# Kernel tuning notes

Hardware: AMD Instinct MI355X
Metric: run time of the kernel (lower is better)

## Reference

```python
import jax, jax.numpy as jnp
import numpy as np

D_MODEL = 1024
N_HEADS = 16
SEQ = 2048
BATCH = 2


def setup_inputs() -> dict:
    key = jax.random.key(0)
    ks = jax.random.split(key, 12)
    s = 1.0 / np.sqrt(D_MODEL)
    return {
        "q_input": jax.random.normal(ks[0], (BATCH, SEQ, D_MODEL), jnp.float32),
        "k_input": jax.random.normal(ks[1], (BATCH, SEQ, D_MODEL), jnp.float32),
        "v_input": jax.random.normal(ks[2], (BATCH, SEQ, D_MODEL), jnp.float32),
        "key_padding_mask": jnp.zeros((BATCH, SEQ), dtype=bool),
        "wq": jax.random.normal(ks[3], (D_MODEL, D_MODEL), jnp.float32) * s,
        "bq": jnp.zeros((D_MODEL,), jnp.float32),
        "wk": jax.random.normal(ks[4], (D_MODEL, D_MODEL), jnp.float32) * s,
        "bk": jnp.zeros((D_MODEL,), jnp.float32),
        "wv": jax.random.normal(ks[5], (D_MODEL, D_MODEL), jnp.float32) * s,
        "bv": jnp.zeros((D_MODEL,), jnp.float32),
        "wo": jax.random.normal(ks[6], (D_MODEL, D_MODEL), jnp.float32) * s,
        "bo": jnp.zeros((D_MODEL,), jnp.float32),
    }


def reference(q_input, k_input, v_input, key_padding_mask, wq, bq, wk, bk, wv, bv, wo, bo):
    B, Lq, _ = q_input.shape
    Lk = k_input.shape[1]
    d_head = D_MODEL // N_HEADS
    # torch Linear: x @ W.T + b
    Q = q_input @ wq.T + bq
    K = k_input @ wk.T + bk
    V = v_input @ wv.T + bv
    # [B, H, L, d_head]
    Qh = Q.reshape(B, Lq, N_HEADS, d_head).transpose(0, 2, 1, 3)
    Kh = K.reshape(B, Lk, N_HEADS, d_head).transpose(0, 2, 1, 3)
    Vh = V.reshape(B, Lk, N_HEADS, d_head).transpose(0, 2, 1, 3)
    scores = jnp.einsum("bhqd,bhkd->bhqk", Qh, Kh) / jnp.sqrt(jnp.float32(d_head))
    # causal mask (use_mask=True)
    causal = jnp.arange(Lk)[None, :] > jnp.arange(Lq)[:, None]  # [Lq, Lk]
    scores = jnp.where(causal[None, None], -jnp.inf, scores)
    # key padding mask [B,1,1,Lk]
    scores = jnp.where(key_padding_mask[:, None, None, :], -jnp.inf, scores)
    # module's global all-inf fallback (scalar condition)
    probs = jnp.where(
        jnp.all(jnp.isinf(scores)),
        jnp.full_like(scores, 1.0 / Lk),
        jax.nn.softmax(scores, axis=-1),
    )
    # dropout is identity in eval mode
    out = jnp.einsum("bhqk,bhkd->bhqd", probs, Vh)
    out = out.transpose(0, 2, 1, 3).reshape(B, Lq, D_MODEL)
    return out @ wo.T + bo
```

## Files before the change

### kernel.cpp

```cpp
#include <hip/hip_runtime.h>
#include <cstdint>
#include <cstddef>

#define DM   1024
#define HEADS 16
#define DH    64
#define SEQL  2048
#define BATCH 2
#define MTOT  (BATCH*SEQL)

typedef __attribute__((ext_vector_type(8))) short short8;
typedef __attribute__((ext_vector_type(4))) float floatx4;

__device__ __forceinline__ unsigned short f2bf(float f) {
  unsigned int u = __float_as_uint(f);
  u = (u + 0x7FFFu + ((u >> 16) & 1u)) >> 16;
  return (unsigned short)u;
}

__device__ __forceinline__ void async_ld16(const void* g, void* l) {
  __builtin_amdgcn_global_load_lds(
      (const __attribute__((address_space(1))) unsigned int*)g,
      (__attribute__((address_space(3))) unsigned int*)l, 16, 0, 0);
}

__global__ void cvt_all(const float* __restrict__ q, const float* __restrict__ k,
                        const float* __restrict__ v, const float* __restrict__ w0,
                        const float* __restrict__ w1, const float* __restrict__ w2,
                        const float* __restrict__ w3,
                        unsigned short* __restrict__ Xq, unsigned short* __restrict__ Xk,
                        unsigned short* __restrict__ Xv, unsigned short* __restrict__ W0,
                        unsigned short* __restrict__ W1, unsigned short* __restrict__ W2,
                        unsigned short* __restrict__ W3) {
  const int bid = blockIdx.x;
  const float* src; unsigned short* dst; int base;
  if (bid < 12288) {
    int seg = bid >> 12;
    base = (bid & 4095) * 1024;
    src = seg == 0 ? q : seg == 1 ? k : v;
    dst = seg == 0 ? Xq : seg == 1 ? Xk : Xv;
  } else {
    int b2 = bid - 12288;
    int seg = b2 >> 10;
    base = (b2 & 1023) * 1024;
    src = seg == 0 ? w0 : seg == 1 ? w1 : seg == 2 ? w2 : w3;
    dst = seg == 0 ? W0 : seg == 1 ? W1 : seg == 2 ? W2 : W3;
  }
  int i = base + threadIdx.x * 4;
  float4 vv = *(const float4*)(src + i);
  ushort4 o;
  o.x = f2bf(vv.x); o.y = f2bf(vv.y); o.z = f2bf(vv.z); o.w = f2bf(vv.w);
  *(ushort4*)(dst + i) = o;
}

__global__ __launch_bounds__(256, 3) void qkv_gemm(
    const unsigned short* Xq, const unsigned short* Xk, const unsigned short* Xv,
    const unsigned short* Wq, const unsigned short* Wk, const unsigned short* Wv,
    const float* bq, const float* bk, const float* bv,
    unsigned short* Qo, unsigned short* Ko, unsigned short* Vo) {
  __shared__ unsigned short As[128 * 64], Bs[128 * 64];
  const unsigned short *A, *Bw; const float* bias; unsigned short* Cout;
  if (blockIdx.z == 0)      { A = Xq; Bw = Wq; bias = bq; Cout = Qo; }
  else if (blockIdx.z == 1) { A = Xk; Bw = Wk; bias = bk; Cout = Ko; }
  else                      { A = Xv; Bw = Wv; bias = bv; Cout = Vo; }

  const int K = DM, N = DM;
  const int m0 = blockIdx.y * 128, n0 = blockIdx.x * 128;
  const int tid  = threadIdx.x;
  const int lane = tid & 63, wvi = tid >> 6;
  const int lq = lane & 15, quad = lane >> 4;
  const int wrow = wvi >> 1, wcol = wvi & 1;

  floatx4 acc[4][4];
  #pragma unroll
  for (int i = 0; i < 4; i++)
    #pragma unroll
    for (int j = 0; j < 4; j++)
      #pragma unroll
      for (int e = 0; e < 4; e++) acc[i][j][e] = 0.0f;

  for (int kt = 0; kt < K; kt += 64) {
    #pragma unroll
    for (int cc = 0; cc < 4; cc++) {
      int c = wvi + cc * 4;
      int e = c * 512 + lane * 8;
      int r = e >> 6, col = e & 63;
      async_ld16(A  + (size_t)(m0 + r) * K + kt + col, As + c * 512);
      async_ld16(Bw + (size_t)(n0 + r) * K + kt + col, Bs + c * 512);
    }
    __syncthreads();
    #pragma unroll
    for (int ks = 0; ks < 64; ks += 32) {
      short8 af[4], bf[4];
      #pragma unroll
      for (int i = 0; i < 4; i++)
        af[i] = *(const short8*)&As[(wrow * 64 + i * 16 + lq) * 64 + ks + quad * 8];
      #pragma unroll
      for (int j = 0; j < 4; j++)
        bf[j] = *(const short8*)&Bs[(wcol * 64 + j * 16 + lq) * 64 + ks + quad * 8];
      #pragma unroll
      for (int i = 0; i < 4; i++)
        #pragma unroll
        for (int j = 0; j < 4; j++)
          acc[i][j] = __builtin_amdgcn_mfma_f32_16x16x32_bf16(af[i], bf[j], acc[i][j], 0, 0, 0);
    }
    __syncthreads();
  }

  #pragma unroll
  for (int i = 0; i < 4; i++) {
    #pragma unroll
    for (int j = 0; j < 4; j++) {
      int colg = n0 + wcol * 64 + j * 16 + lq;
      float bb = bias[colg];
      #pragma unroll
      for (int r = 0; r < 4; r++) {
        int rowg = m0 + wrow * 64 + i * 16 + quad * 4 + r;
        ((unsigned short*)Cout)[(size_t)rowg * N + colg] = f2bf(acc[i][j][r] + bb);
      }
    }
  }
}

__global__ __launch_bounds__(256, 4) void out_gemm(
    const unsigned short* __restrict__ A, const unsigned short* __restrict__ Bw,
    const float* __restrict__ bias, float* __restrict__ C) {
  __shared__ unsigned short As[128 * 64], Bs[64 * 64];
  const int K = DM, N = DM;
  const int m0 = blockIdx.y * 128, n0 = blockIdx.x * 64;
  const int tid  = threadIdx.x;
  const int lane = tid & 63, wvi = tid >> 6;
  const int lq = lane & 15, quad = lane >> 4;
  const int wrow = wvi >> 1, wcol = wvi & 1;

  floatx4 acc[4][2];
  #pragma unroll
  for (int i = 0; i < 4; i++)
    #pragma unroll
    for (int j = 0; j < 2; j++)
      #pragma unroll
      for (int e = 0; e < 4; e++) acc[i][j][e] = 0.0f;

  for (int kt = 0; kt < K; kt += 64) {
    #pragma unroll
    for (int cc = 0; cc < 4; cc++) {
      int c = wvi + cc * 4;
      int e = c * 512 + lane * 8;
      int r = e >> 6, col = e & 63;
      async_ld16(A + (size_t)(m0 + r) * K + kt + col, As + c * 512);
    }
    #pragma unroll
    for (int cc = 0; cc < 2; cc++) {
      int c = wvi + cc * 4;
      int e = c * 512 + lane * 8;
      int r = e >> 6, col = e & 63;
      async_ld16(Bw + (size_t)(n0 + r) * K + kt + col, Bs + c * 512);
    }
    __syncthreads();
    #pragma unroll
    for (int ks = 0; ks < 64; ks += 32) {
      short8 af[4], bf[2];
      #pragma unroll
      for (int i = 0; i < 4; i++)
        af[i] = *(const short8*)&As[(wrow * 64 + i * 16 + lq) * 64 + ks + quad * 8];
      #pragma unroll
      for (int j = 0; j < 2; j++)
        bf[j] = *(const short8*)&Bs[(wcol * 32 + j * 16 + lq) * 64 + ks + quad * 8];
      #pragma unroll
      for (int i = 0; i < 4; i++)
        #pragma unroll
        for (int j = 0; j < 2; j++)
          acc[i][j] = __builtin_amdgcn_mfma_f32_16x16x32_bf16(af[i], bf[j], acc[i][j], 0, 0, 0);
    }
    __syncthreads();
  }

  #pragma unroll
  for (int i = 0; i < 4; i++) {
    #pragma unroll
    for (int j = 0; j < 2; j++) {
      int colg = n0 + wcol * 32 + j * 16 + lq;
      float bb = bias[colg];
      #pragma unroll
      for (int r = 0; r < 4; r++) {
        int rowg = m0 + wrow * 64 + i * 16 + quad * 4 + r;
        C[(size_t)rowg * N + colg] = acc[i][j][r] + bb;
      }
    }
  }
}

__global__ void v_transpose(const unsigned short* __restrict__ Vb,
                            unsigned short* __restrict__ VT) {
  __shared__ unsigned short Ts[64 * 72];
  const int kt = blockIdx.x, h = blockIdx.y, b = blockIdx.z;
  const int tid = threadIdx.x;
  const int krow = tid >> 4, dcol = (tid & 15) * 4;
  const unsigned short* src = Vb + (size_t)(b * SEQL + kt * 64) * DM + h * DH;
  #pragma unroll
  for (int j = 0; j < 4; j++) {
    ushort4 v = *(const ushort4*)(src + (size_t)(j * 16 + krow) * DM + dcol);
    Ts[(dcol + 0) * 72 + j * 16 + krow] = v.x;
    Ts[(dcol + 1) * 72 + j * 16 + krow] = v.y;
    Ts[(dcol + 2) * 72 + j * 16 + krow] = v.z;
    Ts[(dcol + 3) * 72 + j * 16 + krow] = v.w;
  }
  __syncthreads();
  unsigned short* dst = VT + (size_t)((b * HEADS + h) * 32 + kt) * 4096;
  #pragma unroll
  for (int jj = 0; jj < 2; jj++) {
    int e = jj * 256 + tid;
    int drow = e >> 3, koff = (e & 7) * 8;
    *(short8*)(dst + drow * 64 + koff) = *(const short8*)&Ts[drow * 72 + koff];
  }
}

__global__ __launch_bounds__(256, 4) void attn_kernel(
    const unsigned short* __restrict__ Q, const unsigned short* __restrict__ K,
    const unsigned short* __restrict__ VT, const unsigned char* __restrict__ kpm,
    unsigned short* __restrict__ O) {
  __shared__ unsigned short Ks[64 * 72];
  __shared__ unsigned short VTs[64 * 72];
  __shared__ unsigned short Ps[4][16 * 72];

  const int bid = blockIdx.x;
  const int qt = 31 - (bid >> 5);
  const int bh = bid & 31;
  const int h = bh & 15, b = bh >> 4;
  const int tid = threadIdx.x, lane = tid & 63, wvi = tid >> 6;
  const int lq = lane & 15, quad = lane >> 4;
  const size_t bbase = (size_t)b * SEQL * DM;

  const int srow = tid >> 4;
  const int scol = (tid & 15) * 4;

  const unsigned short* kptr = K + bbase + (size_t)h * DH + (size_t)srow * DM + scol;
  const unsigned short* vptr = VT + (size_t)(b * HEADS + h) * 32 * 4096 + srow * 64 + scol;
  const unsigned char*  mptr = kpm + (size_t)b * SEQL + quad * 4;

  const unsigned short* Qrow = Q + bbase + (size_t)(qt * 64 + wvi * 16 + lq) * DM + h * DH;
  const short8 qf0 = *(const short8*)(Qrow + quad * 8);
  const short8 qf1 = *(const short8*)(Qrow + 32 + quad * 8);

  ushort4 kr[4], vr[4];
  unsigned int mr[4];
  #pragma unroll
  for (int j = 0; j < 4; j++) {
    kr[j] = *(const ushort4*)(kptr + (size_t)j * 16 * DM);
    vr[j] = *(const ushort4*)(vptr + j * 1024);
  }
  #pragma unroll
  for (int t = 0; t < 4; t++) mr[t] = *(const unsigned int*)(mptr + t * 16);
  kptr += (size_t)64 * DM; vptr += 4096; mptr += 64;

  float l_run = 0.f;
  floatx4 o[4];
  #pragma unroll
  for (int t = 0; t < 4; t++)
    #pragma unroll
    for (int e = 0; e < 4; e++) o[t][e] = 0.f;

  const float SC = 0.125f * 1.44269504088896f;
  const float C0 = -24.0f * SC;
  const int qg = wvi * 16 + lq;

  auto tile_body = [&](bool diag, const unsigned int* mcur) {
    floatx4 st[4];
    #pragma unroll
    for (int t = 0; t < 4; t++) {
      #pragma unroll
      for (int e = 0; e < 4; e++) st[t][e] = 0.f;
      const short8 a0 = *(const short8*)&Ks[(t * 16 + lq) * 72 + quad * 8];
      const short8 a1 = *(const short8*)&Ks[(t * 16 + lq) * 72 + 32 + quad * 8];
      st[t] = __builtin_amdgcn_mfma_f32_16x16x32_bf16(a0, qf0, st[t], 0, 0, 0);
      st[t] = __builtin_amdgcn_mfma_f32_16x16x32_bf16(a1, qf1, st[t], 0, 0, 0);
    }

    float x[4][4];
    #pragma unroll
    for (int t = 0; t < 4; t++)
      #pragma unroll
      for (int r = 0; r < 4; r++) x[t][r] = st[t][r];

    if (__any((int)((mcur[0] | mcur[1] | mcur[2] | mcur[3]) != 0u))) {
      #pragma unroll
      for (int t = 0; t < 4; t++)
        #pragma unroll
        for (int r = 0; r < 4; r++)
          if ((mcur[t] >> (8 * r)) & 0xffu) x[t][r] = -1e33f;
    }
    if (diag) {
      #pragma unroll
      for (int t = 0; t < 4; t++)
        #pragma unroll
        for (int r = 0; r < 4; r++)
          if (t * 16 + quad * 4 + r > qg) x[t][r] = -1e33f;
    }

    #pragma unroll
    for (int t = 0; t < 4; t++)
      #pragma unroll
      for (int r = 0; r < 4; r++) {
        const float p = exp2f(fmaf(x[t][r], SC, C0));
        x[t][r] = p;
        l_run += p;
      }

    #pragma unroll
    for (int t = 0; t < 4; t++) {
      unsigned int p01 = (__float_as_uint(x[t][1]) & 0xffff0000u) | (__float_as_uint(x[t][0]) >> 16);
      unsigned int p23 = (__float_as_uint(x[t][3]) & 0xffff0000u) | (__float_as_uint(x[t][2]) >> 16);
      *(uint2*)&Ps[wvi][lq * 72 + t * 16 + quad * 4] = make_uint2(p01, p23);
    }

    const short8 pa0 = *(const short8*)&Ps[wvi][lq * 72 + quad * 8];
    const short8 pa1 = *(const short8*)&Ps[wvi][lq * 72 + 32 + quad * 8];
    #pragma unroll
    for (int t = 0; t < 4; t++) {
      const short8 b0 = *(const short8*)&VTs[(t * 16 + lq) * 72 + quad * 8];
      const short8 b1 = *(const short8*)&VTs[(t * 16 + lq) * 72 + 32 + quad * 8];
      o[t] = __builtin_amdgcn_mfma_f32_16x16x32_bf16(pa0, b0, o[t], 0, 0, 0);
      o[t] = __builtin_amdgcn_mfma_f32_16x16x32_bf16(pa1, b1, o[t], 0, 0, 0);
    }
  };

  for (int kt = 0; kt < qt; kt++) {
    __syncthreads();
    #pragma unroll
    for (int j = 0; j < 4; j++) {
      *(ushort4*)&Ks [(j * 16 + srow) * 72 + scol] = kr[j];
      *(ushort4*)&VTs[(j * 16 + srow) * 72 + scol] = vr[j];
    }
    unsigned int mcur[4];
    #pragma unroll
    for (int t = 0; t < 4; t++) mcur[t] = mr[t];
    __syncthreads();

    #pragma unroll
    for (int j = 0; j < 4; j++) {
      kr[j] = *(const ushort4*)(kptr + (size_t)j * 16 * DM);
      vr[j] = *(const ushort4*)(vptr + j * 1024);
    }
    #pragma unroll
    for (int t = 0; t < 4; t++) mr[t] = *(const unsigned int*)(mptr + t * 16);
    kptr += (size_t)64 * DM; vptr += 4096; mptr += 64;

    tile_body(false, mcur);
  }

  __syncthreads();
  #pragma unroll
  for (int j = 0; j < 4; j++) {
    *(ushort4*)&Ks [(j * 16 + srow) * 72 + scol] = kr[j];
    *(ushort4*)&VTs[(j * 16 + srow) * 72 + scol] = vr[j];
  }
  __syncthreads();
  tile_body(true, mr);

  l_run += __shfl_xor(l_run, 16);
  l_run += __shfl_xor(l_run, 32);
  const float li = 1.0f / l_run;
  float linv[4];
  #pragma unroll
  for (int r = 0; r < 4; r++) linv[r] = __shfl(li, quad * 20 + r);
  #pragma unroll
  for (int t = 0; t < 4; t++)
    #pragma unroll
    for (int r = 0; r < 4; r++) {
      const int rowg = qt * 64 + wvi * 16 + quad * 4 + r;
      const int colg = h * 64 + t * 16 + lq;
      O[bbase + (size_t)rowg * DM + colg] = f2bf(o[t][r] * linv[r]);
    }
}

extern "C" void kernel_launch(void* const* d_in, const int* in_sizes, int n_in,
                              void* d_out, int out_size, void* d_ws, size_t ws_size,
                              hipStream_t stream) {
  const float* qin = (const float*)d_in[0];
  const float* kin = (const float*)d_in[1];
  const float* vin = (const float*)d_in[2];
  const unsigned char* kpm = (const unsigned char*)d_in[3];
  const float* wq = (const float*)d_in[4];
  const float* bq = (const float*)d_in[5];
  const float* wk = (const float*)d_in[6];
  const float* bk = (const float*)d_in[7];
  const float* wv = (const float*)d_in[8];
  const float* bv = (const float*)d_in[9];
  const float* wo = (const float*)d_in[10];
  const float* bo = (const float*)d_in[11];

  const size_t XN = (size_t)MTOT * DM;
  const size_t WN = (size_t)DM * DM;
  unsigned short* Xq  = (unsigned short*)d_ws;
  unsigned short* Xk  = Xq  + XN;
  unsigned short* Xv  = Xk  + XN;
  unsigned short* Wqb = Xv  + XN;
  unsigned short* Wkb = Wqb + WN;
  unsigned short* Wvb = Wkb + WN;
  unsigned short* Wob = Wvb + WN;
  unsigned short* Qb  = Wob + WN;
  unsigned short* Kb  = Qb  + XN;
  unsigned short* Vb  = Kb  + XN;
  unsigned short* Ob  = Vb  + XN;
  unsigned short* VTg = Xq;

  cvt_all<<<dim3(16384), 256, 0, stream>>>(qin, kin, vin, wq, wk, wv, wo,
                                           Xq, Xk, Xv, Wqb, Wkb, Wvb, Wob);

  dim3 g1(DM / 128, MTOT / 128, 3);
  qkv_gemm<<<g1, 256, 0, stream>>>(Xq, Xk, Xv, Wqb, Wkb, Wvb, bq, bk, bv, Qb, Kb, Vb);

  v_transpose<<<dim3(SEQL / 64, HEADS, BATCH), 256, 0, stream>>>(Vb, VTg);

  attn_kernel<<<dim3(BATCH * HEADS * (SEQL / 64)), 256, 0, stream>>>(Qb, Kb, VTg, kpm, Ob);

  dim3 g2(DM / 64, MTOT / 128, 1);
  out_gemm<<<g2, 256, 0, stream>>>(Ob, Wob, bo, (float*)d_out);
}
```

Measured before the change: 226.0 us.

## Fuse V transpose into QKV GEMM epilogue and process two query tiles per attention block

The QKV GEMM epilogue now writes V directly in the per-head transposed tile layout, which removes the separate v_transpose kernel and its extra round trip through global memory. The attention kernel now handles 128 query rows per block as two 64-row sub-tiles that share each staged K/V tile, halving K/V reloads and the grid size. Query-tile scheduling is remapped to a 16-tile pairing order. In exchange, the V epilogue does scattered 8-byte stores, and the attention kernel needs more accumulator registers, which may lower occupancy.

```diff
diff --git a/kernel.cpp b/kernel.cpp
--- a/kernel.cpp
+++ b/kernel.cpp
@@ -57,12 +57,12 @@
     const unsigned short* Xq, const unsigned short* Xk, const unsigned short* Xv,
     const unsigned short* Wq, const unsigned short* Wk, const unsigned short* Wv,
     const float* bq, const float* bk, const float* bv,
-    unsigned short* Qo, unsigned short* Ko, unsigned short* Vo) {
+    unsigned short* Qo, unsigned short* Ko, unsigned short* VTo) {
   __shared__ unsigned short As[128 * 64], Bs[128 * 64];
   const unsigned short *A, *Bw; const float* bias; unsigned short* Cout;
   if (blockIdx.z == 0)      { A = Xq; Bw = Wq; bias = bq; Cout = Qo; }
   else if (blockIdx.z == 1) { A = Xk; Bw = Wk; bias = bk; Cout = Ko; }
-  else                      { A = Xv; Bw = Wv; bias = bv; Cout = Vo; }
+  else                      { A = Xv; Bw = Wv; bias = bv; Cout = VTo; }
 
   const int K = DM, N = DM;
   const int m0 = blockIdx.y * 128, n0 = blockIdx.x * 128;
@@ -107,16 +107,38 @@
     __syncthreads();
   }
 
-  #pragma unroll
-  for (int i = 0; i < 4; i++) {
-    #pragma unroll
-    for (int j = 0; j < 4; j++) {
-      int colg = n0 + wcol * 64 + j * 16 + lq;
-      float bb = bias[colg];
-      #pragma unroll
-      for (int r = 0; r < 4; r++) {
-        int rowg = m0 + wrow * 64 + i * 16 + quad * 4 + r;
-        ((unsigned short*)Cout)[(size_t)rowg * N + colg] = f2bf(acc[i][j][r] + bb);
+  if (blockIdx.z == 2) {
+    #pragma unroll
+    for (int i = 0; i < 4; i++) {
+      const int rowg = m0 + wrow * 64 + i * 16 + quad * 4;
+      const int bb  = rowg >> 11;
+      const int kt2 = (rowg & 2047) >> 6;
+      const int k0  = rowg & 63;
+      #pragma unroll
+      for (int j = 0; j < 4; j++) {
+        const int colg = n0 + wcol * 64 + j * 16 + lq;
+        const int h2 = colg >> 6, d2 = colg & 63;
+        const float bb_v = bias[colg];
+        ushort4 w;
+        w.x = f2bf(acc[i][j][0] + bb_v);
+        w.y = f2bf(acc[i][j][1] + bb_v);
+        w.z = f2bf(acc[i][j][2] + bb_v);
+        w.w = f2bf(acc[i][j][3] + bb_v);
+        *(ushort4*)(Cout + (size_t)((bb * HEADS + h2) * 32 + kt2) * 4096 + d2 * 64 + k0) = w;
+      }
+    }
+  } else {
+    #pragma unroll
+    for (int i = 0; i < 4; i++) {
+      #pragma unroll
+      for (int j = 0; j < 4; j++) {
+        int colg = n0 + wcol * 64 + j * 16 + lq;
+        float bb = bias[colg];
+        #pragma unroll
+        for (int r = 0; r < 4; r++) {
+          int rowg = m0 + wrow * 64 + i * 16 + quad * 4 + r;
+          Cout[(size_t)rowg * N + colg] = f2bf(acc[i][j][r] + bb);
+        }
       }
     }
   }
@@ -190,31 +212,6 @@
   }
 }
 
-__global__ void v_transpose(const unsigned short* __restrict__ Vb,
-                            unsigned short* __restrict__ VT) {
-  __shared__ unsigned short Ts[64 * 72];
-  const int kt = blockIdx.x, h = blockIdx.y, b = blockIdx.z;
-  const int tid = threadIdx.x;
-  const int krow = tid >> 4, dcol = (tid & 15) * 4;
-  const unsigned short* src = Vb + (size_t)(b * SEQL + kt * 64) * DM + h * DH;
-  #pragma unroll
-  for (int j = 0; j < 4; j++) {
-    ushort4 v = *(const ushort4*)(src + (size_t)(j * 16 + krow) * DM + dcol);
-    Ts[(dcol + 0) * 72 + j * 16 + krow] = v.x;
-    Ts[(dcol + 1) * 72 + j * 16 + krow] = v.y;
-    Ts[(dcol + 2) * 72 + j * 16 + krow] = v.z;
-    Ts[(dcol + 3) * 72 + j * 16 + krow] = v.w;
-  }
-  __syncthreads();
-  unsigned short* dst = VT + (size_t)((b * HEADS + h) * 32 + kt) * 4096;
-  #pragma unroll
-  for (int jj = 0; jj < 2; jj++) {
-    int e = jj * 256 + tid;
-    int drow = e >> 3, koff = (e & 7) * 8;
-    *(short8*)(dst + drow * 64 + koff) = *(const short8*)&Ts[drow * 72 + koff];
-  }
-}
-
 __global__ __launch_bounds__(256, 4) void attn_kernel(
     const unsigned short* __restrict__ Q, const unsigned short* __restrict__ K,
     const unsigned short* __restrict__ VT, const unsigned char* __restrict__ kpm,
@@ -224,7 +221,8 @@
   __shared__ unsigned short Ps[4][16 * 72];
 
   const int bid = blockIdx.x;
-  const int qt = 31 - (bid >> 5);
+  const int g = bid >> 5;
+  const int qt = (g < 8) ? (15 - g) : (g - 8);
   const int bh = bid & 31;
   const int h = bh & 15, b = bh >> 4;
   const int tid = threadIdx.x, lane = tid & 63, wvi = tid >> 6;
@@ -238,9 +236,14 @@
   const unsigned short* vptr = VT + (size_t)(b * HEADS + h) * 32 * 4096 + srow * 64 + scol;
   const unsigned char*  mptr = kpm + (size_t)b * SEQL + quad * 4;
 
-  const unsigned short* Qrow = Q + bbase + (size_t)(qt * 64 + wvi * 16 + lq) * DM + h * DH;
-  const short8 qf0 = *(const short8*)(Qrow + quad * 8);
-  const short8 qf1 = *(const short8*)(Qrow + 32 + quad * 8);
+  const unsigned short* QrowA = Q + bbase + (size_t)(qt * 128 + wvi * 16 + lq) * DM + h * DH;
+  const short8 qfA0 = *(const short8*)(QrowA + quad * 8);
+  const short8 qfA1 = *(const short8*)(QrowA + 32 + quad * 8);
+  const unsigned short* QrowB = QrowA + (size_t)64 * DM;
+  const short8 qfB0 = *(const short8*)(QrowB + quad * 8);
+  const short8 qfB1 = *(const short8*)(QrowB + 32 + quad * 8);
+
+  const int nk = 2 * qt + 2;
 
   ushort4 kr[4], vr[4];
   unsigned int mr[4];
@@ -253,123 +256,131 @@
   for (int t = 0; t < 4; t++) mr[t] = *(const unsigned int*)(mptr + t * 16);
   kptr += (size_t)64 * DM; vptr += 4096; mptr += 64;
 
-  float l_run = 0.f;
-  floatx4 o[4];
+  float lA = 0.f, lB = 0.f;
+  floatx4 oA[4], oB[4];
   #pragma unroll
   for (int t = 0; t < 4; t++)
     #pragma unroll
-    for (int e = 0; e < 4; e++) o[t][e] = 0.f;
+    for (int e = 0; e < 4; e++) { oA[t][e] = 0.f; oB[t][e] = 0.f; }
 
   const float SC = 0.125f * 1.44269504088896f;
   const float C0 = -24.0f * SC;
   const int qg = wvi * 16 + lq;
 
-  auto tile_body = [&](bool diag, const unsigned int* mcur) {
-    floatx4 st[4];
+  for (int kt = 0; kt < nk; kt++) {
+    __syncthreads();
+    #pragma unroll
+    for (int j = 0; j < 4; j++) {
+      *(ushort4*)&Ks [(j * 16 + srow) * 72 + scol] = kr[j];
+      *(ushort4*)&VTs[(j * 16 + srow) * 72 + scol] = vr[j];
+    }
+    unsigned int mcur[4];
+    #pragma unroll
+    for (int t = 0; t < 4; t++) mcur[t] = mr[t];
+    __syncthreads();
+
+    if (kt + 1 < nk) {
+      #pragma unroll
+      for (int j = 0; j < 4; j++) {
+        kr[j] = *(const ushort4*)(kptr + (size_t)j * 16 * DM);
+        vr[j] = *(const ushort4*)(vptr + j * 1024);
+      }
+      #pragma unroll
+      for (int t = 0; t < 4; t++) mr[t] = *(const unsigned int*)(mptr + t * 16);
+      kptr += (size_t)64 * DM; vptr += 4096; mptr += 64;
+    }
+
+    floatx4 sA[4], sB[4];
     #pragma unroll
     for (int t = 0; t < 4; t++) {
       #pragma unroll
-      for (int e = 0; e < 4; e++) st[t][e] = 0.f;
+      for (int e = 0; e < 4; e++) { sA[t][e] = 0.f; sB[t][e] = 0.f; }
       const short8 a0 = *(const short8*)&Ks[(t * 16 + lq) * 72 + quad * 8];
       const short8 a1 = *(const short8*)&Ks[(t * 16 + lq) * 72 + 32 + quad * 8];
-      st[t] = __builtin_amdgcn_mfma_f32_16x16x32_bf16(a0, qf0, st[t], 0, 0, 0);
-      st[t] = __builtin_amdgcn_mfma_f32_16x16x32_bf16(a1, qf1, st[t], 0, 0, 0);
-    }
-
-    float x[4][4];
+      sA[t] = __builtin_amdgcn_mfma_f32_16x16x32_bf16(a0, qfA0, sA[t], 0, 0, 0);
+      sA[t] = __builtin_amdgcn_mfma_f32_16x16x32_bf16(a1, qfA1, sA[t], 0, 0, 0);
+      sB[t] = __builtin_amdgcn_mfma_f32_16x16x32_bf16(a0, qfB0, sB[t], 0, 0, 0);
+      sB[t] = __builtin_amdgcn_mfma_f32_16x16x32_bf16(a1, qfB1, sB[t], 0, 0, 0);
+    }
+
+    if (__any((int)((mcur[0] | mcur[1] | mcur[2] | mcur[3]) != 0u))) {
+      #pragma unroll
+      for (int t = 0; t < 4; t++)
+        #pragma unroll
+        for (int r = 0; r < 4; r++)
+          if ((mcur[t] >> (8 * r)) & 0xffu) { sA[t][r] = -1e33f; sB[t][r] = -1e33f; }
+    }
+    if (kt >= 2 * qt) {
+      const int offA = qg + (2 * qt - kt) * 64;
+      #pragma unroll
+      for (int t = 0; t < 4; t++)
+        #pragma unroll
+        for (int r = 0; r < 4; r++)
+          if (t * 16 + quad * 4 + r > offA) sA[t][r] = -1e33f;
+    }
+    if (kt == 2 * qt + 1) {
+      #pragma unroll
+      for (int t = 0; t < 4; t++)
+        #pragma unroll
+        for (int r = 0; r < 4; r++)
+          if (t * 16 + quad * 4 + r > qg) sB[t][r] = -1e33f;
+    }
+
     #pragma unroll
     for (int t = 0; t < 4; t++)
       #pragma unroll
-      for (int r = 0; r < 4; r++) x[t][r] = st[t][r];
-
-    if (__any((int)((mcur[0] | mcur[1] | mcur[2] | mcur[3]) != 0u))) {
-      #pragma unroll
-      for (int t = 0; t < 4; t++)
-        #pragma unroll
-        for (int r = 0; r < 4; r++)
-          if ((mcur[t] >> (8 * r)) & 0xffu) x[t][r] = -1e33f;
-    }
-    if (diag) {
-      #pragma unroll
-      for (int t = 0; t < 4; t++)
-        #pragma unroll
-        for (int r = 0; r < 4; r++)
-          if (t * 16 + quad * 4 + r > qg) x[t][r] = -1e33f;
-    }
-
-    #pragma unroll
-    for (int t = 0; t < 4; t++)
-      #pragma unroll
       for (int r = 0; r < 4; r++) {
-        const float p = exp2f(fmaf(x[t][r], SC, C0));
-        x[t][r] = p;
-        l_run += p;
+        const float pA = exp2f(fmaf(sA[t][r], SC, C0));
+        const float pB = exp2f(fmaf(sB[t][r], SC, C0));
+        sA[t][r] = pA; lA += pA;
+        sB[t][r] = pB; lB += pB;
       }
 
     #pragma unroll
     for (int t = 0; t < 4; t++) {
-      unsigned int p01 = (__float_as_uint(x[t][1]) & 0xffff0000u) | (__float_as_uint(x[t][0]) >> 16);
-      unsigned int p23 = (__float_as_uint(x[t][3]) & 0xffff0000u) | (__float_as_uint(x[t][2]) >> 16);
+      unsigned int p01 = (__float_as_uint(sA[t][1]) & 0xffff0000u) | (__float_as_uint(sA[t][0]) >> 16);
+      unsigned int p23 = (__float_as_uint(sA[t][3]) & 0xffff0000u) | (__float_as_uint(sA[t][2]) >> 16);
       *(uint2*)&Ps[wvi][lq * 72 + t * 16 + quad * 4] = make_uint2(p01, p23);
     }
-
-    const short8 pa0 = *(const short8*)&Ps[wvi][lq * 72 + quad * 8];
-    const short8 pa1 = *(const short8*)&Ps[wvi][lq * 72 + 32 + quad * 8];
+    const short8 paA0 = *(const short8*)&Ps[wvi][lq * 72 + quad * 8];
+    const short8 paA1 = *(const short8*)&Ps[wvi][lq * 72 + 32 + quad * 8];
+    #pragma unroll
+    for (int t = 0; t < 4; t++) {
+      unsigned int p01 = (__float_as_uint(sB[t][1]) & 0xffff0000u) | (__float_as_uint(sB[t][0]) >> 16);
+      unsigned int p23 = (__float_as_uint(sB[t][3]) & 0xffff0000u) | (__float_as_uint(sB[t][2]) >> 16);
+      *(uint2*)&Ps[wvi][lq * 72 + t * 16 + quad * 4] = make_uint2(p01, p23);
+    }
+    const short8 paB0 = *(const short8*)&Ps[wvi][lq * 72 + quad * 8];
+    const short8 paB1 = *(const short8*)&Ps[wvi][lq * 72 + 32 + quad * 8];
+
     #pragma unroll
     for (int t = 0; t < 4; t++) {
       const short8 b0 = *(const short8*)&VTs[(t * 16 + lq) * 72 + quad * 8];
       const short8 b1 = *(const short8*)&VTs[(t * 16 + lq) * 72 + 32 + quad * 8];
-      o[t] = __builtin_amdgcn_mfma_f32_16x16x32_bf16(pa0, b0, o[t], 0, 0, 0);
-      o[t] = __builtin_amdgcn_mfma_f32_16x16x32_bf16(pa1, b1, o[t], 0, 0, 0);
-    }
-  };
-
-  for (int kt = 0; kt < qt; kt++) {
-    __syncthreads();
-    #pragma unroll
-    for (int j = 0; j < 4; j++) {
-      *(ushort4*)&Ks [(j * 16 + srow) * 72 + scol] = kr[j];
-      *(ushort4*)&VTs[(j * 16 + srow) * 72 + scol] = vr[j];
-    }
-    unsigned int mcur[4];
-    #pragma unroll
-    for (int t = 0; t < 4; t++) mcur[t] = mr[t];
-    __syncthreads();
-
-    #pragma unroll
-    for (int j = 0; j < 4; j++) {
-      kr[j] = *(const ushort4*)(kptr + (size_t)j * 16 * DM);
-      vr[j] = *(const ushort4*)(vptr + j * 1024);
-    }
-    #pragma unroll
-    for (int t = 0; t < 4; t++) mr[t] = *(const unsigned int*)(mptr + t * 16);
-    kptr += (size_t)64 * DM; vptr += 4096; mptr += 64;
-
-    tile_body(false, mcur);
-  }
-
-  __syncthreads();
-  #pragma unroll
-  for (int j = 0; j < 4; j++) {
-    *(ushort4*)&Ks [(j * 16 + srow) * 72 + scol] = kr[j];
-    *(ushort4*)&VTs[(j * 16 + srow) * 72 + scol] = vr[j];
-  }
-  __syncthreads();
-  tile_body(true, mr);
-
-  l_run += __shfl_xor(l_run, 16);
-  l_run += __shfl_xor(l_run, 32);
-  const float li = 1.0f / l_run;
-  float linv[4];
-  #pragma unroll
-  for (int r = 0; r < 4; r++) linv[r] = __shfl(li, quad * 20 + r);
+      oA[t] = __builtin_amdgcn_mfma_f32_16x16x32_bf16(paA0, b0, oA[t], 0, 0, 0);
+      oA[t] = __builtin_amdgcn_mfma_f32_16x16x32_bf16(paA1, b1, oA[t], 0, 0, 0);
+      oB[t] = __builtin_amdgcn_mfma_f32_16x16x32_bf16(paB0, b0, oB[t], 0, 0, 0);
+      oB[t] = __builtin_amdgcn_mfma_f32_16x16x32_bf16(paB1, b1, oB[t], 0, 0, 0);
+    }
+  }
+
+  lA += __shfl_xor(lA, 16); lA += __shfl_xor(lA, 32);
+  lB += __shfl_xor(lB, 16); lB += __shfl_xor(lB, 32);
+  const float liA = 1.0f / lA, liB = 1.0f / lB;
+  float invA[4], invB[4];
+  #pragma unroll
+  for (int r = 0; r < 4; r++) {
+    invA[r] = __shfl(liA, quad * 20 + r);
+    invB[r] = __shfl(liB, quad * 20 + r);
+  }
   #pragma unroll
   for (int t = 0; t < 4; t++)
     #pragma unroll
     for (int r = 0; r < 4; r++) {
-      const int rowg = qt * 64 + wvi * 16 + quad * 4 + r;
+      const int rowA = qt * 128 + wvi * 16 + quad * 4 + r;
       const int colg = h * 64 + t * 16 + lq;
-      O[bbase + (size_t)rowg * DM + colg] = f2bf(o[t][r] * linv[r]);
+      O[bbase + (size_t)rowA * DM + colg] = f2bf(oA[t][r] * invA[r]);
+      O[bbase + (size_t)(rowA + 64) * DM + colg] = f2bf(oB[t][r] * invB[r]);
     }
 }
 
@@ -400,19 +411,16 @@
   unsigned short* Wob = Wvb + WN;
   unsigned short* Qb  = Wob + WN;
   unsigned short* Kb  = Qb  + XN;
-  unsigned short* Vb  = Kb  + XN;
-  unsigned short* Ob  = Vb  + XN;
-  unsigned short* VTg = Xq;
+  unsigned short* VTg = Kb  + XN;
+  unsigned short* Ob  = VTg + XN;
 
   cvt_all<<<dim3(16384), 256, 0, stream>>>(qin, kin, vin, wq, wk, wv, wo,
                                            Xq, Xk, Xv, Wqb, Wkb, Wvb, Wob);
 
   dim3 g1(DM / 128, MTOT / 128, 3);
-  qkv_gemm<<<g1, 256, 0, stream>>>(Xq, Xk, Xv, Wqb, Wkb, Wvb, bq, bk, bv, Qb, Kb, Vb);
-
-  v_transpose<<<dim3(SEQL / 64, HEADS, BATCH), 256, 0, stream>>>(Vb, VTg);
-
-  attn_kernel<<<dim3(BATCH * HEADS * (SEQL / 64)), 256, 0, stream>>>(Qb, Kb, VTg, kpm, Ob);
+  qkv_gemm<<<g1, 256, 0, stream>>>(Xq, Xk, Xv, Wqb, Wkb, Wvb, bq, bk, bv, Qb, Kb, VTg);
+
+  attn_kernel<<<dim3(BATCH * HEADS * (SEQL / 128)), 256, 0, stream>>>(Qb, Kb, VTg, kpm, Ob);
 
   dim3 g2(DM / 64, MTOT / 128, 1);
   out_gemm<<<g2, 256, 0, stream>>>(Ob, Wob, bo, (float*)d_out);
```

Result: slower. 247.6 us (+9.6%).

## Fuse activation bf16 conversion and V transpose into QKV GEMM

Applied to the files above, without the earlier changes.

Removes the separate fp32-to-bf16 conversion pass over the Q/K/V activations. The QKV GEMM now loads fp32 rows directly, rounds them to bf16 in registers and writes them to shared memory. The V projection epilogue writes straight into the transposed per-head tile layout, so the v_transpose kernel is dropped. This cuts global memory traffic and two launches, but A-tile loads become synchronous register loads instead of async LDS loads, and the rounding changes from round-to-nearest-even to round-half-up.

```diff
diff --git a/kernel.cpp b/kernel.cpp
--- a/kernel.cpp
+++ b/kernel.cpp
@@ -24,28 +24,15 @@
       (__attribute__((address_space(3))) unsigned int*)l, 16, 0, 0);
 }
 
-__global__ void cvt_all(const float* __restrict__ q, const float* __restrict__ k,
-                        const float* __restrict__ v, const float* __restrict__ w0,
-                        const float* __restrict__ w1, const float* __restrict__ w2,
-                        const float* __restrict__ w3,
-                        unsigned short* __restrict__ Xq, unsigned short* __restrict__ Xk,
-                        unsigned short* __restrict__ Xv, unsigned short* __restrict__ W0,
-                        unsigned short* __restrict__ W1, unsigned short* __restrict__ W2,
-                        unsigned short* __restrict__ W3) {
+__global__ void cvt_w(const float* __restrict__ w0, const float* __restrict__ w1,
+                      const float* __restrict__ w2, const float* __restrict__ w3,
+                      unsigned short* __restrict__ W0, unsigned short* __restrict__ W1,
+                      unsigned short* __restrict__ W2, unsigned short* __restrict__ W3) {
   const int bid = blockIdx.x;
-  const float* src; unsigned short* dst; int base;
-  if (bid < 12288) {
-    int seg = bid >> 12;
-    base = (bid & 4095) * 1024;
-    src = seg == 0 ? q : seg == 1 ? k : v;
-    dst = seg == 0 ? Xq : seg == 1 ? Xk : Xv;
-  } else {
-    int b2 = bid - 12288;
-    int seg = b2 >> 10;
-    base = (b2 & 1023) * 1024;
-    src = seg == 0 ? w0 : seg == 1 ? w1 : seg == 2 ? w2 : w3;
-    dst = seg == 0 ? W0 : seg == 1 ? W1 : seg == 2 ? W2 : W3;
-  }
+  const int seg = bid >> 10;
+  const int base = (bid & 1023) * 1024;
+  const float* src = seg == 0 ? w0 : seg == 1 ? w1 : seg == 2 ? w2 : w3;
+  unsigned short* dst = seg == 0 ? W0 : seg == 1 ? W1 : seg == 2 ? W2 : W3;
   int i = base + threadIdx.x * 4;
   float4 vv = *(const float4*)(src + i);
   ushort4 o;
@@ -54,15 +41,15 @@
 }
 
 __global__ __launch_bounds__(256, 3) void qkv_gemm(
-    const unsigned short* Xq, const unsigned short* Xk, const unsigned short* Xv,
+    const float* Xq, const float* Xk, const float* Xv,
     const unsigned short* Wq, const unsigned short* Wk, const unsigned short* Wv,
     const float* bq, const float* bk, const float* bv,
-    unsigned short* Qo, unsigned short* Ko, unsigned short* Vo) {
+    unsigned short* Qo, unsigned short* Ko, unsigned short* VTo) {
   __shared__ unsigned short As[128 * 64], Bs[128 * 64];
-  const unsigned short *A, *Bw; const float* bias; unsigned short* Cout;
+  const float* A; const unsigned short* Bw; const float* bias; unsigned short* Cout;
   if (blockIdx.z == 0)      { A = Xq; Bw = Wq; bias = bq; Cout = Qo; }
   else if (blockIdx.z == 1) { A = Xk; Bw = Wk; bias = bk; Cout = Ko; }
-  else                      { A = Xv; Bw = Wv; bias = bv; Cout = Vo; }
+  else                      { A = Xv; Bw = Wv; bias = bv; Cout = VTo; }
 
   const int K = DM, N = DM;
   const int m0 = blockIdx.y * 128, n0 = blockIdx.x * 128;
@@ -71,6 +58,9 @@
   const int lq = lane & 15, quad = lane >> 4;
   const int wrow = wvi >> 1, wcol = wvi & 1;
 
+  const int arow8 = lane >> 3;
+  const int acol  = (lane & 7) * 8;
+
   floatx4 acc[4][4];
   #pragma unroll
   for (int i = 0; i < 4; i++)
@@ -85,8 +75,29 @@
       int c = wvi + cc * 4;
       int e = c * 512 + lane * 8;
       int r = e >> 6, col = e & 63;
-      async_ld16(A  + (size_t)(m0 + r) * K + kt + col, As + c * 512);
       async_ld16(Bw + (size_t)(n0 + r) * K + kt + col, Bs + c * 512);
+    }
+    #pragma unroll
+    for (int cc = 0; cc < 4; cc++) {
+      int c = wvi + cc * 4;
+      int r = c * 8 + arow8;
+      const float* src = A + (size_t)(m0 + r) * K + kt + acol;
+      float4 f0 = *(const float4*)src;
+      float4 f1 = *(const float4*)(src + 4);
+      unsigned int a0 = __float_as_uint(f0.x) + 0x8000u;
+      unsigned int a1 = __float_as_uint(f0.y) + 0x8000u;
+      unsigned int a2 = __float_as_uint(f0.z) + 0x8000u;
+      unsigned int a3 = __float_as_uint(f0.w) + 0x8000u;
+      unsigned int a4 = __float_as_uint(f1.x) + 0x8000u;
+      unsigned int a5 = __float_as_uint(f1.y) + 0x8000u;
+      unsigned int a6 = __float_as_uint(f1.z) + 0x8000u;
+      unsigned int a7 = __float_as_uint(f1.w) + 0x8000u;
+      uint4 w;
+      w.x = (a1 & 0xffff0000u) | (a0 >> 16);
+      w.y = (a3 & 0xffff0000u) | (a2 >> 16);
+      w.z = (a5 & 0xffff0000u) | (a4 >> 16);
+      w.w = (a7 & 0xffff0000u) | (a6 >> 16);
+      *(uint4*)&As[c * 512 + lane * 8] = w;
     }
     __syncthreads();
     #pragma unroll
@@ -107,16 +118,38 @@
     __syncthreads();
   }
 
-  #pragma unroll
-  for (int i = 0; i < 4; i++) {
-    #pragma unroll
-    for (int j = 0; j < 4; j++) {
-      int colg = n0 + wcol * 64 + j * 16 + lq;
-      float bb = bias[colg];
-      #pragma unroll
-      for (int r = 0; r < 4; r++) {
-        int rowg = m0 + wrow * 64 + i * 16 + quad * 4 + r;
-        ((unsigned short*)Cout)[(size_t)rowg * N + colg] = f2bf(acc[i][j][r] + bb);
+  if (blockIdx.z == 2) {
+    #pragma unroll
+    for (int i = 0; i < 4; i++) {
+      const int rowg = m0 + wrow * 64 + i * 16 + quad * 4;
+      const int bb  = rowg >> 11;
+      const int kt2 = (rowg & 2047) >> 6;
+      const int k0  = rowg & 63;
+      #pragma unroll
+      for (int j = 0; j < 4; j++) {
+        const int colg = n0 + wcol * 64 + j * 16 + lq;
+        const int h2 = colg >> 6, d2 = colg & 63;
+        const float bb_v = bias[colg];
+        ushort4 w;
+        w.x = f2bf(acc[i][j][0] + bb_v);
+        w.y = f2bf(acc[i][j][1] + bb_v);
+        w.z = f2bf(acc[i][j][2] + bb_v);
+        w.w = f2bf(acc[i][j][3] + bb_v);
+        *(ushort4*)(Cout + (size_t)((bb * HEADS + h2) * 32 + kt2) * 4096 + d2 * 64 + k0) = w;
+      }
+    }
+  } else {
+    #pragma unroll
+    for (int i = 0; i < 4; i++) {
+      #pragma unroll
+      for (int j = 0; j < 4; j++) {
+        int colg = n0 + wcol * 64 + j * 16 + lq;
+        float bb = bias[colg];
+        #pragma unroll
+        for (int r = 0; r < 4; r++) {
+          int rowg = m0 + wrow * 64 + i * 16 + quad * 4 + r;
+          Cout[(size_t)rowg * N + colg] = f2bf(acc[i][j][r] + bb);
+        }
       }
     }
   }
@@ -187,31 +220,6 @@
         C[(size_t)rowg * N + colg] = acc[i][j][r] + bb;
       }
     }
-  }
-}
-
-__global__ void v_transpose(const unsigned short* __restrict__ Vb,
-                            unsigned short* __restrict__ VT) {
-  __shared__ unsigned short Ts[64 * 72];
-  const int kt = blockIdx.x, h = blockIdx.y, b = blockIdx.z;
-  const int tid = threadIdx.x;
-  const int krow = tid >> 4, dcol = (tid & 15) * 4;
-  const unsigned short* src = Vb + (size_t)(b * SEQL + kt * 64) * DM + h * DH;
-  #pragma unroll
-  for (int j = 0; j < 4; j++) {
-    ushort4 v = *(const ushort4*)(src + (size_t)(j * 16 + krow) * DM + dcol);
-    Ts[(dcol + 0) * 72 + j * 16 + krow] = v.x;
-    Ts[(dcol + 1) * 72 + j * 16 + krow] = v.y;
-    Ts[(dcol + 2) * 72 + j * 16 + krow] = v.z;
-    Ts[(dcol + 3) * 72 + j * 16 + krow] = v.w;
-  }
-  __syncthreads();
-  unsigned short* dst = VT + (size_t)((b * HEADS + h) * 32 + kt) * 4096;
-  #pragma unroll
-  for (int jj = 0; jj < 2; jj++) {
-    int e = jj * 256 + tid;
-    int drow = e >> 3, koff = (e & 7) * 8;
-    *(short8*)(dst + drow * 64 + koff) = *(const short8*)&Ts[drow * 72 + koff];
   }
 }
 
@@ -391,26 +399,19 @@
 
   const size_t XN = (size_t)MTOT * DM;
   const size_t WN = (size_t)DM * DM;
-  unsigned short* Xq  = (unsigned short*)d_ws;
-  unsigned short* Xk  = Xq  + XN;
-  unsigned short* Xv  = Xk  + XN;
-  unsigned short* Wqb = Xv  + XN;
+  unsigned short* Wqb = (unsigned short*)d_ws;
   unsigned short* Wkb = Wqb + WN;
   unsigned short* Wvb = Wkb + WN;
   unsigned short* Wob = Wvb + WN;
   unsigned short* Qb  = Wob + WN;
   unsigned short* Kb  = Qb  + XN;
-  unsigned short* Vb  = Kb  + XN;
-  unsigned short* Ob  = Vb  + XN;
-  unsigned short* VTg = Xq;
-
-  cvt_all<<<dim3(16384), 256, 0, stream>>>(qin, kin, vin, wq, wk, wv, wo,
-                                           Xq, Xk, Xv, Wqb, Wkb, Wvb, Wob);
+  unsigned short* VTg = Kb  + XN;
+  unsigned short* Ob  = VTg + XN;
+
+  cvt_w<<<dim3(4096), 256, 0, stream>>>(wq, wk, wv, wo, Wqb, Wkb, Wvb, Wob);
 
   dim3 g1(DM / 128, MTOT / 128, 3);
-  qkv_gemm<<<g1, 256, 0, stream>>>(Xq, Xk, Xv, Wqb, Wkb, Wvb, bq, bk, bv, Qb, Kb, Vb);
-
-  v_transpose<<<dim3(SEQL / 64, HEADS, BATCH), 256, 0, stream>>>(Vb, VTg);
+  qkv_gemm<<<g1, 256, 0, stream>>>(qin, kin, vin, Wqb, Wkb, Wvb, bq, bk, bv, Qb, Kb, VTg);
 
   attn_kernel<<<dim3(BATCH * HEADS * (SEQL / 64)), 256, 0, stream>>>(Qb, Kb, VTg, kpm, Ob);
 
```

Result: slower. 238.2 us (+5.4%).

## Fuse V transpose into QKV GEMM epilogue and retile output GEMM

Applied to the files above, without the earlier changes.

The QKV GEMM now writes V directly in the per-head transposed tile layout the attention kernel expects, which removes the separate v_transpose kernel and its extra read and write of V. The output projection GEMM is retiled from 128x64 to 64x128 blocks, with each wave owning 16 rows across all 128 columns. The fused epilogue writes 4-element chunks with a strided scatter, which may coalesce less well than row-major stores.

```diff
diff --git a/kernel.cpp b/kernel.cpp
--- a/kernel.cpp
+++ b/kernel.cpp
@@ -57,12 +57,12 @@
     const unsigned short* Xq, const unsigned short* Xk, const unsigned short* Xv,
     const unsigned short* Wq, const unsigned short* Wk, const unsigned short* Wv,
     const float* bq, const float* bk, const float* bv,
-    unsigned short* Qo, unsigned short* Ko, unsigned short* Vo) {
+    unsigned short* Qo, unsigned short* Ko, unsigned short* VTo) {
   __shared__ unsigned short As[128 * 64], Bs[128 * 64];
   const unsigned short *A, *Bw; const float* bias; unsigned short* Cout;
   if (blockIdx.z == 0)      { A = Xq; Bw = Wq; bias = bq; Cout = Qo; }
   else if (blockIdx.z == 1) { A = Xk; Bw = Wk; bias = bk; Cout = Ko; }
-  else                      { A = Xv; Bw = Wv; bias = bv; Cout = Vo; }
+  else                      { A = Xv; Bw = Wv; bias = bv; Cout = VTo; }
 
   const int K = DM, N = DM;
   const int m0 = blockIdx.y * 128, n0 = blockIdx.x * 128;
@@ -107,16 +107,38 @@
     __syncthreads();
   }
 
-  #pragma unroll
-  for (int i = 0; i < 4; i++) {
-    #pragma unroll
-    for (int j = 0; j < 4; j++) {
-      int colg = n0 + wcol * 64 + j * 16 + lq;
-      float bb = bias[colg];
-      #pragma unroll
-      for (int r = 0; r < 4; r++) {
-        int rowg = m0 + wrow * 64 + i * 16 + quad * 4 + r;
-        ((unsigned short*)Cout)[(size_t)rowg * N + colg] = f2bf(acc[i][j][r] + bb);
+  if (blockIdx.z == 2) {
+    #pragma unroll
+    for (int i = 0; i < 4; i++) {
+      const int rowg = m0 + wrow * 64 + i * 16 + quad * 4;
+      const int bb  = rowg >> 11;
+      const int kt2 = (rowg & 2047) >> 6;
+      const int k0  = rowg & 63;
+      #pragma unroll
+      for (int j = 0; j < 4; j++) {
+        const int colg = n0 + wcol * 64 + j * 16 + lq;
+        const int h2 = colg >> 6, d2 = colg & 63;
+        const float bb_v = bias[colg];
+        ushort4 w;
+        w.x = f2bf(acc[i][j][0] + bb_v);
+        w.y = f2bf(acc[i][j][1] + bb_v);
+        w.z = f2bf(acc[i][j][2] + bb_v);
+        w.w = f2bf(acc[i][j][3] + bb_v);
+        *(ushort4*)(Cout + (size_t)((bb * HEADS + h2) * 32 + kt2) * 4096 + d2 * 64 + k0) = w;
+      }
+    }
+  } else {
+    #pragma unroll
+    for (int i = 0; i < 4; i++) {
+      #pragma unroll
+      for (int j = 0; j < 4; j++) {
+        int colg = n0 + wcol * 64 + j * 16 + lq;
+        float bb = bias[colg];
+        #pragma unroll
+        for (int r = 0; r < 4; r++) {
+          int rowg = m0 + wrow * 64 + i * 16 + quad * 4 + r;
+          Cout[(size_t)rowg * N + colg] = f2bf(acc[i][j][r] + bb);
+        }
       }
     }
   }
@@ -125,93 +147,56 @@
 __global__ __launch_bounds__(256, 4) void out_gemm(
     const unsigned short* __restrict__ A, const unsigned short* __restrict__ Bw,
     const float* __restrict__ bias, float* __restrict__ C) {
-  __shared__ unsigned short As[128 * 64], Bs[64 * 64];
+  __shared__ unsigned short As[64 * 64], Bs[128 * 64];
   const int K = DM, N = DM;
-  const int m0 = blockIdx.y * 128, n0 = blockIdx.x * 64;
+  const int m0 = blockIdx.y * 64, n0 = blockIdx.x * 128;
   const int tid  = threadIdx.x;
   const int lane = tid & 63, wvi = tid >> 6;
   const int lq = lane & 15, quad = lane >> 4;
-  const int wrow = wvi >> 1, wcol = wvi & 1;
-
-  floatx4 acc[4][2];
-  #pragma unroll
-  for (int i = 0; i < 4; i++)
-    #pragma unroll
-    for (int j = 0; j < 2; j++)
-      #pragma unroll
-      for (int e = 0; e < 4; e++) acc[i][j][e] = 0.0f;
+
+  floatx4 acc[8];
+  #pragma unroll
+  for (int j = 0; j < 8; j++)
+    #pragma unroll
+    for (int e = 0; e < 4; e++) acc[j][e] = 0.0f;
 
   for (int kt = 0; kt < K; kt += 64) {
+    #pragma unroll
+    for (int cc = 0; cc < 2; cc++) {
+      int c = wvi + cc * 4;
+      int e = c * 512 + lane * 8;
+      int r = e >> 6, col = e & 63;
+      async_ld16(A + (size_t)(m0 + r) * K + kt + col, As + c * 512);
+    }
     #pragma unroll
     for (int cc = 0; cc < 4; cc++) {
       int c = wvi + cc * 4;
       int e = c * 512 + lane * 8;
       int r = e >> 6, col = e & 63;
-      async_ld16(A + (size_t)(m0 + r) * K + kt + col, As + c * 512);
-    }
-    #pragma unroll
-    for (int cc = 0; cc < 2; cc++) {
-      int c = wvi + cc * 4;
-      int e = c * 512 + lane * 8;
-      int r = e >> 6, col = e & 63;
       async_ld16(Bw + (size_t)(n0 + r) * K + kt + col, Bs + c * 512);
     }
     __syncthreads();
     #pragma unroll
     for (int ks = 0; ks < 64; ks += 32) {
-      short8 af[4], bf[2];
-      #pragma unroll
-      for (int i = 0; i < 4; i++)
-        af[i] = *(const short8*)&As[(wrow * 64 + i * 16 + lq) * 64 + ks + quad * 8];
-      #pragma unroll
-      for (int j = 0; j < 2; j++)
-        bf[j] = *(const short8*)&Bs[(wcol * 32 + j * 16 + lq) * 64 + ks + quad * 8];
-      #pragma unroll
-      for (int i = 0; i < 4; i++)
-        #pragma unroll
-        for (int j = 0; j < 2; j++)
-          acc[i][j] = __builtin_amdgcn_mfma_f32_16x16x32_bf16(af[i], bf[j], acc[i][j], 0, 0, 0);
-    }
-    __syncthreads();
-  }
-
-  #pragma unroll
-  for (int i = 0; i < 4; i++) {
-    #pragma unroll
-    for (int j = 0; j < 2; j++) {
-      int colg = n0 + wcol * 32 + j * 16 + lq;
-      float bb = bias[colg];
-      #pragma unroll
-      for (int r = 0; r < 4; r++) {
-        int rowg = m0 + wrow * 64 + i * 16 + quad * 4 + r;
-        C[(size_t)rowg * N + colg] = acc[i][j][r] + bb;
+      const short8 af = *(const short8*)&As[(wvi * 16 + lq) * 64 + ks + quad * 8];
+      #pragma unroll
+      for (int j = 0; j < 8; j++) {
+        const short8 bf = *(const short8*)&Bs[(j * 16 + lq) * 64 + ks + quad * 8];
+        acc[j] = __builtin_amdgcn_mfma_f32_16x16x32_bf16(af, bf, acc[j], 0, 0, 0);
       }
     }
-  }
-}
-
-__global__ void v_transpose(const unsigned short* __restrict__ Vb,
-                            unsigned short* __restrict__ VT) {
-  __shared__ unsigned short Ts[64 * 72];
-  const int kt = blockIdx.x, h = blockIdx.y, b = blockIdx.z;
-  const int tid = threadIdx.x;
-  const int krow = tid >> 4, dcol = (tid & 15) * 4;
-  const unsigned short* src = Vb + (size_t)(b * SEQL + kt * 64) * DM + h * DH;
-  #pragma unroll
-  for (int j = 0; j < 4; j++) {
-    ushort4 v = *(const ushort4*)(src + (size_t)(j * 16 + krow) * DM + dcol);
-    Ts[(dcol + 0) * 72 + j * 16 + krow] = v.x;
-    Ts[(dcol + 1) * 72 + j * 16 + krow] = v.y;
-    Ts[(dcol + 2) * 72 + j * 16 + krow] = v.z;
-    Ts[(dcol + 3) * 72 + j * 16 + krow] = v.w;
-  }
-  __syncthreads();
-  unsigned short* dst = VT + (size_t)((b * HEADS + h) * 32 + kt) * 4096;
-  #pragma unroll
-  for (int jj = 0; jj < 2; jj++) {
-    int e = jj * 256 + tid;
-    int drow = e >> 3, koff = (e & 7) * 8;
-    *(short8*)(dst + drow * 64 + koff) = *(const short8*)&Ts[drow * 72 + koff];
+    __syncthreads();
+  }
+
+  #pragma unroll
+  for (int j = 0; j < 8; j++) {
+    const int colg = n0 + j * 16 + lq;
+    const float bb = bias[colg];
+    #pragma unroll
+    for (int r = 0; r < 4; r++) {
+      const int rowg = m0 + wvi * 16 + quad * 4 + r;
+      C[(size_t)rowg * N + colg] = acc[j][r] + bb;
+    }
   }
 }
 
@@ -400,20 +385,17 @@
   unsigned short* Wob = Wvb + WN;
   unsigned short* Qb  = Wob + WN;
   unsigned short* Kb  = Qb  + XN;
-  unsigned short* Vb  = Kb  + XN;
-  unsigned short* Ob  = Vb  + XN;
-  unsigned short* VTg = Xq;
+  unsigned short* VTg = Kb  + XN;
+  unsigned short* Ob  = VTg + XN;
 
   cvt_all<<<dim3(16384), 256, 0, stream>>>(qin, kin, vin, wq, wk, wv, wo,
                                            Xq, Xk, Xv, Wqb, Wkb, Wvb, Wob);
 
   dim3 g1(DM / 128, MTOT / 128, 3);
-  qkv_gemm<<<g1, 256, 0, stream>>>(Xq, Xk, Xv, Wqb, Wkb, Wvb, bq, bk, bv, Qb, Kb, Vb);
-
-  v_transpose<<<dim3(SEQL / 64, HEADS, BATCH), 256, 0, stream>>>(Vb, VTg);
+  qkv_gemm<<<g1, 256, 0, stream>>>(Xq, Xk, Xv, Wqb, Wkb, Wvb, bq, bk, bv, Qb, Kb, VTg);
 
   attn_kernel<<<dim3(BATCH * HEADS * (SEQL / 64)), 256, 0, stream>>>(Qb, Kb, VTg, kpm, Ob);
 
-  dim3 g2(DM / 64, MTOT / 128, 1);
+  dim3 g2(DM / 128, MTOT / 64, 1);
   out_gemm<<<g2, 256, 0, stream>>>(Ob, Wob, bo, (float*)d_out);
 }
```

Measured after the change: 225.9 us. No clear change (-0.0%).
